# Kernel tuning notes

Hardware: AMD Instinct MI355X
Metric: run time of the kernel (lower is better)

## Reference

```python
import jax, jax.numpy as jnp
import numpy as np

EPS = 1e-5
K = 3  # neighborhood kernel size per axis


def setup_inputs() -> dict:
    key = jax.random.key(0)
    ks = jax.random.split(key, 12)
    C, F, G = 128, 512, 8
    s = 0.02
    d = {}
    d["x"] = jax.random.normal(ks[0], (1, C, 32, 32, 32), jnp.float32)
    d["qkv_w"] = s * jax.random.normal(ks[1], (3 * C, C), jnp.float32)
    d["qkv_b"] = jnp.zeros((3 * C,), jnp.float32)
    d["proj_w"] = s * jax.random.normal(ks[2], (C, C), jnp.float32)
    d["proj_b"] = jnp.zeros((C,), jnp.float32)
    d["rpb"] = s * jax.random.normal(ks[3], (G, 2 * K - 1, 2 * K - 1, 2 * K - 1), jnp.float32)
    d["w1"] = s * jax.random.normal(ks[4], (C, F), jnp.float32)
    d["b1"] = jnp.zeros((F,), jnp.float32)
    d["w2"] = s * jax.random.normal(ks[5], (F, C), jnp.float32)
    d["b2"] = jnp.zeros((C,), jnp.float32)
    return d


def _nb_idx(n, k):
    # NATTEN-style clamped window: neighborhood start clipped so the full
    # k-window stays in-bounds -> every query has exactly k neighbors per axis.
    pos = jnp.arange(n)
    start = jnp.clip(pos - (k // 2), 0, n - k)
    return start[:, None] + jnp.arange(k)[None, :]  # (n, k)


def _inorm(x):
    # InstanceNorm3d, affine=False: normalize each (b, c) over spatial dims
    m = jnp.mean(x, axis=(2, 3, 4), keepdims=True)
    v = jnp.var(x, axis=(2, 3, 4), keepdims=True)
    return (x - m) * jax.lax.rsqrt(v + EPS)


def _forward(x, qkv_w, qkv_b, proj_w, proj_b, rpb, w1, b1, w2, b2):
    b, c, h, w, z = x.shape
    G = rpb.shape[0]
    D = c // G

    # --- SAM: 3D neighborhood self-attention ---
    qkv = jnp.einsum('bchwz,oc->bohwz', x, qkv_w) + qkv_b[None, :, None, None, None]
    q, k_, v = jnp.split(qkv, 3, axis=1)
    q = q.reshape(b, G, D, h, w, z)
    k_ = k_.reshape(b, G, D, h, w, z)
    v = v.reshape(b, G, D, h, w, z)

    ih, iw, iz = _nb_idx(h, K), _nb_idx(w, K), _nb_idx(z, K)  # (h,K),(w,K),(z,K)
    IH = ih[:, None, None, :, None, None]
    IW = iw[None, :, None, None, :, None]
    IZ = iz[None, None, :, None, None, :]
    # gathered neighbors: (b, G, D, h, w, z, K, K, K) -> (..., K^3)
    knb = k_[:, :, :, IH, IW, IZ].reshape(b, G, D, h, w, z, K ** 3)
    vnb = v[:, :, :, IH, IW, IZ].reshape(b, G, D, h, w, z, K ** 3)

    # relative-position-bias indices in [0, 2K-2]
    rh = ih - jnp.arange(h)[:, None] + (K - 1)
    rw = iw - jnp.arange(w)[:, None] + (K - 1)
    rz = iz - jnp.arange(z)[:, None] + (K - 1)
    RH = rh[:, None, None, :, None, None]
    RW = rw[None, :, None, None, :, None]
    RZ = rz[None, None, :, None, None, :]
    rpbg = rpb[:, RH, RW, RZ].reshape(G, h, w, z, K ** 3)

    scale = D ** -0.5
    attn = jnp.einsum('bgdhwz,bgdhwzk->bghwzk', q, knb) * scale + rpbg[None]
    attn = jax.nn.softmax(attn, axis=-1)
    sam = jnp.einsum('bghwzk,bgdhwzk->bgdhwz', attn, vnb).reshape(b, c, h, w, z)
    sam = jnp.einsum('bchwz,oc->bohwz', sam, proj_w) + proj_b[None, :, None, None, None]

    # --- norm_in + FFN (tokens = h*w*z) + norm_out + residual + maxpool ---
    xn = _inorm(sam)
    t = xn.reshape(b, c, -1).transpose(0, 2, 1)  # (b, N, c)
    t = t + (jnp.matmul(jax.nn.relu(jnp.matmul(t, w1) + b1), w2) + b2)
    xn = _inorm(t.transpose(0, 2, 1).reshape(b, c, h, w, z))
    skip = xn + x
    down = jax.lax.reduce_window(skip, -jnp.inf, jax.lax.max,
                                 (1, 1, 2, 2, 2), (1, 1, 2, 2, 2), 'VALID')
    return down, skip


def reference(x, qkv_w, qkv_b, proj_w, proj_b, rpb, w1, b1, w2, b2):
    return _forward(x, qkv_w, qkv_b, proj_w, proj_b, rpb, w1, b1, w2, b2)
```

## Files before the change

### kernel.cpp

```cpp
#include <hip/hip_runtime.h>

#define NSP 32768
#define EPS 1e-5f

typedef __attribute__((ext_vector_type(8))) __bf16 bf16x8;
typedef __attribute__((ext_vector_type(4))) float f32x4;
typedef __attribute__((ext_vector_type(2))) float f32x2;
typedef __attribute__((ext_vector_type(8))) unsigned short us8;
typedef __attribute__((ext_vector_type(2))) unsigned short us2;

union U8 { us8 u; bf16x8 b; };

__device__ __forceinline__ unsigned short f2bf(float f) {
    unsigned u = __float_as_uint(f);
    u += 0x7fff + ((u >> 16) & 1);
    return (unsigned short)(u >> 16);
}
__device__ __forceinline__ float bf2f(unsigned short h) {
    return __uint_as_float(((unsigned)h) << 16);
}

__device__ __forceinline__ void prep_range(
    const float* __restrict__ W, int sO, int sC, int ntk,
    unsigned short* __restrict__ Wsw, int i)
{
    int tile = i >> 13;
    int s = i & 8191;
    int r = s >> 6;
    int byte = (s & 63) << 1;
    int ub = byte ^ ((r & 7) << 4);
    int c = ub >> 4;
    int j = (ub >> 1) & 7;
    int ob = tile / ntk;
    int ks = tile - ob * ntk;
    Wsw[i] = f2bf(W[(ob * 128 + r) * sO + (ks * 64 + c * 8 + j) * sC]);
}

__global__ __launch_bounds__(256) void prep_all(
    const float* __restrict__ qkv_w, const float* __restrict__ proj_w,
    const float* __restrict__ w1, const float* __restrict__ w2,
    unsigned short* __restrict__ qkv_sw, unsigned short* __restrict__ proj_sw,
    unsigned short* __restrict__ w1_sw, unsigned short* __restrict__ w2_sw,
    float* __restrict__ sums)
{
    int bid = blockIdx.x, tid = threadIdx.x;
    if (bid < 192)       prep_range(qkv_w, 128, 1, 2, qkv_sw, bid * 256 + tid);
    else if (bid < 256)  prep_range(proj_w, 128, 1, 2, proj_sw, (bid - 192) * 256 + tid);
    else if (bid < 512)  prep_range(w1, 1, 512, 2, w1_sw, (bid - 256) * 256 + tid);
    else if (bid < 768)  prep_range(w2, 1, 128, 8, w2_sw, (bid - 512) * 256 + tid);
    else { sums[tid] = 0.f; sums[tid + 256] = 0.f; }
}

template<int BN, int XMODE, int OMODE>
__global__ __launch_bounds__(256) void gemm_mfma(
    const unsigned short* __restrict__ Wsw,
    const void* __restrict__ X,
    const float* __restrict__ bias,
    const unsigned short* __restrict__ resid,
    const f32x2* __restrict__ table,
    void* __restrict__ Out,
    int K, int do_relu, int rw)
{
    constexpr int NF = BN / 32;
    constexpr int BCH = BN / 32;
    __shared__ __align__(16) unsigned short smem[8192 + BN * 64];
    unsigned short* Asm = smem;
    unsigned short* Bsm = smem + 8192;
    const int tid  = threadIdx.x;
    const int lane = tid & 63;
    const int wid  = tid >> 6;
    const int wr   = wid >> 1, wc = wid & 1;
    const int n0   = blockIdx.x * BN;
    const int o0   = blockIdx.y << 7;
    const int nk   = K >> 6;

    f32x4 acc[4][NF];
    #pragma unroll
    for (int m = 0; m < 4; ++m)
        #pragma unroll
        for (int n = 0; n < NF; ++n)
            acc[m][n] = (f32x4){0.f, 0.f, 0.f, 0.f};

    const int r  = (BN == 128) ? (tid & 127) : (tid & 63);
    const int kh = (BN == 128) ? (tid >> 7)  : (tid >> 6);

    us8 a_pre[4];
    us8 b_pre[BCH];
    int b_c[BCH];
    #pragma unroll
    for (int i = 0; i < BCH; ++i)
        b_c[i] = (BN == 128) ? (((((r >> 5) + i) & 3) << 1) + kh)
                             : (((((r >> 4) + i) & 1) << 2) + kh);

    auto load_tile = [&](int ks) {
        const char* gbase = (const char*)(Wsw + (size_t)(blockIdx.y * nk + ks) * 8192);
        #pragma unroll
        for (int i = 0; i < 4; ++i)
            a_pre[i] = *(const us8*)(gbase + i * 4096 + tid * 16);
        #pragma unroll
        for (int i = 0; i < BCH; ++i) {
            int c = b_c[i];
            int kb = (ks << 6) + (c << 3);
            us8 bv;
            if (XMODE == 0) {
                const float* xp = (const float*)X + (size_t)kb * NSP + n0 + r;
                #pragma unroll
                for (int j = 0; j < 8; ++j) bv[j] = f2bf(xp[(size_t)j * NSP]);
            } else if (XMODE == 2) {
                bv = *(const us8*)((const unsigned short*)X + (size_t)(n0 + r) * rw + kb);
            } else {
                const unsigned short* xp = (const unsigned short*)X + (size_t)kb * NSP + n0 + r;
                #pragma unroll
                for (int j = 0; j < 8; ++j) {
                    f32x2 t = table[kb + j];
                    bv[j] = f2bf((bf2f(xp[(size_t)j * NSP]) - t.x) * t.y);
                }
            }
            b_pre[i] = bv;
        }
    };
    auto store_tile = [&]() {
        #pragma unroll
        for (int i = 0; i < 4; ++i)
            *(us8*)((char*)Asm + i * 4096 + tid * 16) = a_pre[i];
        #pragma unroll
        for (int i = 0; i < BCH; ++i) {
            int off = (r << 7) + ((b_c[i] << 4) ^ ((r & 7) << 4));
            *(us8*)((char*)Bsm + off) = b_pre[i];
        }
    };

    load_tile(0);
    store_tile();
    __syncthreads();

    for (int ks = 0; ks < nk; ++ks) {
        if (ks + 1 < nk) load_tile(ks + 1);
        #pragma unroll
        for (int ki = 0; ki < 2; ++ki) {
            bf16x8 af[4], bfr[NF];
            int chunk = (ki << 2) + (lane >> 4);
            #pragma unroll
            for (int m = 0; m < 4; ++m) {
                int row = (wr << 6) + (m << 4) + (lane & 15);
                int off = (row << 7) + ((chunk << 4) ^ ((row & 7) << 4));
                U8 t; t.u = *(const us8*)((const char*)Asm + off);
                af[m] = t.b;
            }
            #pragma unroll
            for (int n = 0; n < NF; ++n) {
                int row = wc * (BN / 2) + (n << 4) + (lane & 15);
                int off = (row << 7) + ((chunk << 4) ^ ((row & 7) << 4));
                U8 t; t.u = *(const us8*)((const char*)Bsm + off);
                bfr[n] = t.b;
            }
            #pragma unroll
            for (int m = 0; m < 4; ++m)
                #pragma unroll
                for (int n = 0; n < NF; ++n)
                    acc[m][n] = __builtin_amdgcn_mfma_f32_16x16x32_bf16(af[m], bfr[n], acc[m][n], 0, 0, 0);
        }
        if (ks + 1 < nk) {
            __syncthreads();
            store_tile();
            __syncthreads();
        }
    }

    if (OMODE == 2 || OMODE == 3) {
        __syncthreads();
        unsigned short* Wt = smem + (wid << 12);
        #pragma unroll
        for (int m = 0; m < 4; ++m)
            #pragma unroll
            for (int reg = 0; reg < 4; ++reg) {
                int ol = (m << 4) + ((lane >> 4) << 2) + reg;
                float b = bias[o0 + (wr << 6) + ol];
                #pragma unroll
                for (int n = 0; n < NF; ++n) {
                    int cl = (n << 4) + (lane & 15);
                    float v = acc[m][n][reg] + b;
                    if (do_relu) v = fmaxf(v, 0.f);
                    Wt[ol * 64 + (cl ^ ((ol & 7) << 3))] = f2bf(v);
                }
            }
        const int d = lane & 15, coff = lane >> 4;
        unsigned short* O = (unsigned short*)Out;
        #pragma unroll
        for (int go = 0; go < 4; ++go) {
            #pragma unroll
            for (int cc = 0; cc < 16; ++cc) {
                int cl = (cc << 2) + coff;
                int ol = (go << 4) + d;
                unsigned short v = Wt[ol * 64 + (cl ^ ((ol & 7) << 3))];
                size_t idx;
                if (OMODE == 2) {
                    int g = (wr << 2) + go;
                    idx = ((size_t)((blockIdx.y << 3) + g) * NSP + n0 + (wc << 6) + cl) * 16 + d;
                } else {
                    idx = (size_t)(n0 + (wc << 6) + cl) * rw + o0 + (wr << 6) + (go << 4) + d;
                }
                O[idx] = v;
            }
        }
        return;
    }

    #pragma unroll
    for (int m = 0; m < 4; ++m) {
        #pragma unroll
        for (int reg = 0; reg < 4; ++reg) {
            int o = o0 + (wr << 6) + (m << 4) + ((lane >> 4) << 2) + reg;
            float b = bias[o];
            f32x2 rt = resid ? table[o] : (f32x2){0.f, 1.f};
            #pragma unroll
            for (int n = 0; n < NF; ++n) {
                int col = n0 + wc * (BN / 2) + (n << 4) + (lane & 15);
                size_t oi = (size_t)o * NSP + col;
                float v = acc[m][n][reg] + b;
                if (resid) v += (bf2f(resid[oi]) - rt.x) * rt.y;
                if (do_relu) v = fmaxf(v, 0.f);
                ((unsigned short*)Out)[oi] = f2bf(v);
            }
        }
    }
}

__global__ __launch_bounds__(256) void attn_kernel(
    const unsigned short* __restrict__ qkvT, const float* __restrict__ rpb,
    unsigned short* __restrict__ samT)
{
    const int g = blockIdx.y;
    const int n = blockIdx.x * 256 + threadIdx.x;
    const int h = n >> 10, w = (n >> 5) & 31, z = n & 31;
    const int ih0 = min(max(h - 1, 0), 29);
    const int iw0 = min(max(w - 1, 0), 29);
    const int iz0 = min(max(z - 1, 0), 29);

    const us8* qp = (const us8*)(qkvT + ((size_t)g * NSP + n) * 16);
    const unsigned short* kb = qkvT + (size_t)(8 + g) * NSP * 16;
    const unsigned short* vb = qkvT + (size_t)(16 + g) * NSP * 16;

    float q[16];
    {
        us8 q0 = qp[0], q1 = qp[1];
        #pragma unroll
        for (int j = 0; j < 8; ++j) { q[j] = bf2f(q0[j]); q[8 + j] = bf2f(q1[j]); }
    }

    float logits[27];
    int idx = 0;
    #pragma unroll
    for (int kh = 0; kh < 3; ++kh)
    #pragma unroll
    for (int kw = 0; kw < 3; ++kw)
    #pragma unroll
    for (int kz = 0; kz < 3; ++kz) {
        int hh = ih0 + kh, ww = iw0 + kw, zz = iz0 + kz;
        int nb = (hh << 10) + (ww << 5) + zz;
        const us8* kp = (const us8*)(kb + (size_t)nb * 16);
        us8 k0 = kp[0], k1 = kp[1];
        float s = 0.f;
        #pragma unroll
        for (int j = 0; j < 8; ++j) s += q[j] * bf2f(k0[j]);
        #pragma unroll
        for (int j = 0; j < 8; ++j) s += q[8 + j] * bf2f(k1[j]);
        int rh = hh - h + 2, rw = ww - w + 2, rz = zz - z + 2;
        logits[idx++] = s * 0.25f + rpb[g * 125 + rh * 25 + rw * 5 + rz];
    }

    float mx = -1e30f;
    #pragma unroll
    for (int i = 0; i < 27; ++i) mx = fmaxf(mx, logits[i]);
    float sum = 0.f;
    #pragma unroll
    for (int i = 0; i < 27; ++i) { logits[i] = __expf(logits[i] - mx); sum += logits[i]; }
    float inv = 1.f / sum;

    float o[16] = {};
    idx = 0;
    #pragma unroll
    for (int kh = 0; kh < 3; ++kh)
    #pragma unroll
    for (int kw = 0; kw < 3; ++kw)
    #pragma unroll
    for (int kz = 0; kz < 3; ++kz) {
        int nb = ((ih0 + kh) << 10) + ((iw0 + kw) << 5) + (iz0 + kz);
        const us8* vp = (const us8*)(vb + (size_t)nb * 16);
        us8 v0 = vp[0], v1 = vp[1];
        float a = logits[idx++] * inv;
        #pragma unroll
        for (int j = 0; j < 8; ++j) { o[j] += a * bf2f(v0[j]); o[8 + j] += a * bf2f(v1[j]); }
    }
    us8 o0v, o1v;
    #pragma unroll
    for (int j = 0; j < 8; ++j) { o0v[j] = f2bf(o[j]); o1v[j] = f2bf(o[8 + j]); }
    us8* op = (us8*)(samT + (size_t)n * 128 + g * 16);
    op[0] = o0v; op[1] = o1v;
}

__global__ __launch_bounds__(256) void inorm_partial_bf16(
    const unsigned short* __restrict__ in, float* __restrict__ sums)
{
    const int c = blockIdx.x >> 3, seg = blockIdx.x & 7;
    const us8* p = (const us8*)(in + (size_t)c * NSP + seg * 4096);
    float s = 0.f, ss = 0.f;
    #pragma unroll
    for (int i = 0; i < 2; ++i) {
        us8 v = p[threadIdx.x + i * 256];
        #pragma unroll
        for (int j = 0; j < 8; ++j) { float f = bf2f(v[j]); s += f; ss += f * f; }
    }
    for (int off = 32; off > 0; off >>= 1) {
        s  += __shfl_down(s, off);
        ss += __shfl_down(ss, off);
    }
    __shared__ float red[2][4];
    int wid = threadIdx.x >> 6;
    if ((threadIdx.x & 63) == 0) { red[0][wid] = s; red[1][wid] = ss; }
    __syncthreads();
    if (threadIdx.x == 0) {
        atomicAdd(&sums[c * 2],     red[0][0] + red[0][1] + red[0][2] + red[0][3]);
        atomicAdd(&sums[c * 2 + 1], red[1][0] + red[1][1] + red[1][2] + red[1][3]);
    }
}

__global__ void finalize_sums(const float* __restrict__ sums, f32x2* __restrict__ table)
{
    int c = threadIdx.x;
    float m = sums[c * 2] * (1.f / NSP);
    float var = sums[c * 2 + 1] * (1.f / NSP) - m * m;
    table[c] = (f32x2){m, rsqrtf(var + EPS)};
}

__global__ __launch_bounds__(256) void inorm_skip_pool(
    const unsigned short* __restrict__ t2, const float* __restrict__ x,
    const float* __restrict__ sums,
    float* __restrict__ skip, float* __restrict__ down)
{
    int m = blockIdx.x * 256 + threadIdx.x;
    int c = m >> 12;
    int r = m & 4095;
    int oh = r >> 8, ow = (r >> 4) & 15, oz = r & 15;
    float mean = sums[c * 2] * (1.f / NSP);
    float inv = rsqrtf(sums[c * 2 + 1] * (1.f / NSP) - mean * mean + EPS);
    size_t base = (size_t)c * NSP + oh * 2048 + ow * 64 + oz * 2;
    float mx = -1e30f;
    #pragma unroll
    for (int dh = 0; dh < 2; ++dh)
    #pragma unroll
    for (int dw = 0; dw < 2; ++dw) {
        size_t a = base + dh * 1024 + dw * 32;
        us2 tv = *(const us2*)(t2 + a);
        f32x2 xv = *(const f32x2*)(x + a);
        f32x2 sv;
        sv.x = (bf2f(tv.x) - mean) * inv + xv.x;
        sv.y = (bf2f(tv.y) - mean) * inv + xv.y;
        *(f32x2*)(skip + a) = sv;
        mx = fmaxf(mx, fmaxf(sv.x, sv.y));
    }
    down[m] = mx;
}

extern "C" void kernel_launch(void* const* d_in, const int* in_sizes, int n_in,
                              void* d_out, int out_size, void* d_ws, size_t ws_size,
                              hipStream_t stream)
{
    const float* x      = (const float*)d_in[0];
    const float* qkv_w  = (const float*)d_in[1];
    const float* qkv_b  = (const float*)d_in[2];
    const float* proj_w = (const float*)d_in[3];
    const float* proj_b = (const float*)d_in[4];
    const float* rpb    = (const float*)d_in[5];
    const float* w1     = (const float*)d_in[6];
    const float* b1     = (const float*)d_in[7];
    const float* w2     = (const float*)d_in[8];
    const float* b2     = (const float*)d_in[9];

    float* out  = (float*)d_out;
    float* down = out;
    float* skip = out + 524288;

    unsigned short* wb      = (unsigned short*)d_out;
    unsigned short* qkv_sw  = wb;
    unsigned short* proj_sw = wb + 49152;
    unsigned short* w1_sw   = wb + 65536;
    unsigned short* w2_sw   = wb + 131072;

    char* ws = (char*)d_ws;
    const size_t MB = 1u << 20;
    unsigned short* qkvT    = (unsigned short*)(ws);
    unsigned short* samT    = (unsigned short*)(ws + 24 * MB);
    unsigned short* yb      = (unsigned short*)(ws + 32 * MB);
    unsigned short* hiddenT = (unsigned short*)(ws);
    unsigned short* t2b     = (unsigned short*)(ws + 48 * MB);
    float*          sums    = (float*)(ws + 72 * MB);
    f32x2*          table1  = (f32x2*)(ws + 72 * MB + 4096);
    float* sums1 = sums;
    float* sums2 = sums + 256;

    prep_all<<<769, 256, 0, stream>>>(qkv_w, proj_w, w1, w2,
                                      qkv_sw, proj_sw, w1_sw, w2_sw, sums);

    gemm_mfma<128, 0, 2><<<dim3(256, 3), 256, 0, stream>>>(
        qkv_sw, x, qkv_b, nullptr, nullptr, qkvT, 128, 0, 0);
    attn_kernel<<<dim3(128, 8), 256, 0, stream>>>(qkvT, rpb, samT);
    gemm_mfma<64, 2, 1><<<dim3(512, 1), 256, 0, stream>>>(
        proj_sw, samT, proj_b, nullptr, nullptr, yb, 128, 0, 128);
    inorm_partial_bf16<<<1024, 256, 0, stream>>>(yb, sums1);
    finalize_sums<<<1, 128, 0, stream>>>(sums1, table1);
    gemm_mfma<128, 3, 3><<<dim3(256, 4), 256, 0, stream>>>(
        w1_sw, yb, b1, nullptr, table1, hiddenT, 128, 1, 512);
    gemm_mfma<64, 2, 1><<<dim3(512, 1), 256, 0, stream>>>(
        w2_sw, hiddenT, b2, yb, table1, t2b, 512, 0, 512);
    inorm_partial_bf16<<<1024, 256, 0, stream>>>(t2b, sums2);
    inorm_skip_pool<<<2048, 256, 0, stream>>>(t2b, x, sums2, skip, down);
}
```

Baseline: 191.0 us.

## Fuse FFN up and down projections into one MLP kernel keeping hidden in LDS

Replaces the two FFN GEMM launches and the finalize_sums kernel with a single mlp_kernel. Each block handles 64 tokens, normalizes its input tile in LDS, and loops over four 128-wide hidden chunks, computing relu(W1·x) into LDS and accumulating W2·h in registers, then adds the residual. This removes the global write and read of the 32768x512 bf16 hidden tensor and two launches. In exchange, each block reloads all weights from global or L2 memory, runs more sync barriers, and uses 64 KB of LDS, which may limit occupancy.

```diff
diff --git a/kernel.cpp b/kernel.cpp
--- a/kernel.cpp
+++ b/kernel.cpp
@@ -56,10 +56,8 @@
     const unsigned short* __restrict__ Wsw,
     const void* __restrict__ X,
     const float* __restrict__ bias,
-    const unsigned short* __restrict__ resid,
-    const f32x2* __restrict__ table,
     void* __restrict__ Out,
-    int K, int do_relu, int rw)
+    int K, int rw)
 {
     constexpr int NF = BN / 32;
     constexpr int BCH = BN / 32;
@@ -106,15 +104,8 @@
                 const float* xp = (const float*)X + (size_t)kb * NSP + n0 + r;
                 #pragma unroll
                 for (int j = 0; j < 8; ++j) bv[j] = f2bf(xp[(size_t)j * NSP]);
-            } else if (XMODE == 2) {
+            } else {
                 bv = *(const us8*)((const unsigned short*)X + (size_t)(n0 + r) * rw + kb);
-            } else {
-                const unsigned short* xp = (const unsigned short*)X + (size_t)kb * NSP + n0 + r;
-                #pragma unroll
-                for (int j = 0; j < 8; ++j) {
-                    f32x2 t = table[kb + j];
-                    bv[j] = f2bf((bf2f(xp[(size_t)j * NSP]) - t.x) * t.y);
-                }
             }
             b_pre[i] = bv;
         }
@@ -167,7 +158,7 @@
         }
     }
 
-    if (OMODE == 2 || OMODE == 3) {
+    if (BN == 128 && OMODE == 2) {
         __syncthreads();
         unsigned short* Wt = smem + (wid << 12);
         #pragma unroll
@@ -179,27 +170,20 @@
                 #pragma unroll
                 for (int n = 0; n < NF; ++n) {
                     int cl = (n << 4) + (lane & 15);
-                    float v = acc[m][n][reg] + b;
-                    if (do_relu) v = fmaxf(v, 0.f);
-                    Wt[ol * 64 + (cl ^ ((ol & 7) << 3))] = f2bf(v);
+                    Wt[ol * 64 + (cl ^ ((ol & 7) << 3))] = f2bf(acc[m][n][reg] + b);
                 }
             }
         const int d = lane & 15, coff = lane >> 4;
         unsigned short* O = (unsigned short*)Out;
         #pragma unroll
         for (int go = 0; go < 4; ++go) {
+            int g = (wr << 2) + go;
             #pragma unroll
             for (int cc = 0; cc < 16; ++cc) {
                 int cl = (cc << 2) + coff;
                 int ol = (go << 4) + d;
                 unsigned short v = Wt[ol * 64 + (cl ^ ((ol & 7) << 3))];
-                size_t idx;
-                if (OMODE == 2) {
-                    int g = (wr << 2) + go;
-                    idx = ((size_t)((blockIdx.y << 3) + g) * NSP + n0 + (wc << 6) + cl) * 16 + d;
-                } else {
-                    idx = (size_t)(n0 + (wc << 6) + cl) * rw + o0 + (wr << 6) + (go << 4) + d;
-                }
+                size_t idx = ((size_t)((blockIdx.y << 3) + g) * NSP + n0 + (wc << 6) + cl) * 16 + d;
                 O[idx] = v;
             }
         }
@@ -212,18 +196,170 @@
         for (int reg = 0; reg < 4; ++reg) {
             int o = o0 + (wr << 6) + (m << 4) + ((lane >> 4) << 2) + reg;
             float b = bias[o];
-            f32x2 rt = resid ? table[o] : (f32x2){0.f, 1.f};
             #pragma unroll
             for (int n = 0; n < NF; ++n) {
                 int col = n0 + wc * (BN / 2) + (n << 4) + (lane & 15);
                 size_t oi = (size_t)o * NSP + col;
-                float v = acc[m][n][reg] + b;
-                if (resid) v += (bf2f(resid[oi]) - rt.x) * rt.y;
-                if (do_relu) v = fmaxf(v, 0.f);
-                ((unsigned short*)Out)[oi] = f2bf(v);
-            }
-        }
-    }
+                ((unsigned short*)Out)[oi] = f2bf(acc[m][n][reg] + b);
+            }
+        }
+    }
+}
+
+__global__ __launch_bounds__(256) void mlp_kernel(
+    const unsigned short* __restrict__ w1_sw,
+    const unsigned short* __restrict__ w2_sw,
+    const unsigned short* __restrict__ yb,
+    const float* __restrict__ sums1,
+    const float* __restrict__ b1, const float* __restrict__ b2,
+    unsigned short* __restrict__ t2b)
+{
+    __shared__ __align__(16) unsigned short smem[32768];
+    unsigned short* Asm = smem;
+    unsigned short* Xs  = smem + 16384;
+    unsigned short* Hs  = smem + 24576;
+    const int tid  = threadIdx.x;
+    const int lane = tid & 63;
+    const int wid  = tid >> 6;
+    const int wr   = wid >> 1, wc = wid & 1;
+    const int n0   = blockIdx.x << 6;
+
+    {
+        const int r = tid & 63, q = tid >> 6;
+        #pragma unroll
+        for (int i = 0; i < 4; ++i) {
+            int ch = q + (i << 2);
+            int k0 = ch << 3;
+            us8 bv;
+            #pragma unroll
+            for (int j = 0; j < 8; ++j) {
+                int k = k0 + j;
+                float mmean = sums1[k * 2] * (1.f / NSP);
+                float inv = rsqrtf(sums1[k * 2 + 1] * (1.f / NSP) - mmean * mmean + EPS);
+                bv[j] = f2bf((bf2f(yb[(size_t)k * NSP + n0 + r]) - mmean) * inv);
+            }
+            int off = ((ch >> 3) << 13) + (r << 7) + (((ch & 7) << 4) ^ ((r & 7) << 4));
+            *(us8*)((char*)Xs + off) = bv;
+        }
+    }
+    __syncthreads();
+
+    f32x4 acc2[4][2];
+    #pragma unroll
+    for (int m = 0; m < 4; ++m)
+        #pragma unroll
+        for (int n = 0; n < 2; ++n)
+            acc2[m][n] = (f32x4){0.f, 0.f, 0.f, 0.f};
+
+    for (int c = 0; c < 4; ++c) {
+        if (c) __syncthreads();
+        {
+            const char* g = (const char*)(w1_sw + (size_t)c * 16384);
+            #pragma unroll
+            for (int i = 0; i < 8; ++i)
+                *(us8*)((char*)Asm + i * 4096 + tid * 16) = *(const us8*)(g + i * 4096 + tid * 16);
+        }
+        __syncthreads();
+        f32x4 accH[4][2];
+        #pragma unroll
+        for (int m = 0; m < 4; ++m)
+            #pragma unroll
+            for (int n = 0; n < 2; ++n)
+                accH[m][n] = (f32x4){0.f, 0.f, 0.f, 0.f};
+        #pragma unroll
+        for (int kt = 0; kt < 2; ++kt) {
+            #pragma unroll
+            for (int ki = 0; ki < 2; ++ki) {
+                int chunk = (ki << 2) + (lane >> 4);
+                bf16x8 af[4], bfr[2];
+                #pragma unroll
+                for (int m = 0; m < 4; ++m) {
+                    int row = (wr << 6) + (m << 4) + (lane & 15);
+                    int off = (kt << 14) + (row << 7) + ((chunk << 4) ^ ((row & 7) << 4));
+                    U8 t; t.u = *(const us8*)((const char*)Asm + off);
+                    af[m] = t.b;
+                }
+                #pragma unroll
+                for (int n = 0; n < 2; ++n) {
+                    int row = (wc << 5) + (n << 4) + (lane & 15);
+                    int off = (kt << 13) + (row << 7) + ((chunk << 4) ^ ((row & 7) << 4));
+                    U8 t; t.u = *(const us8*)((const char*)Xs + off);
+                    bfr[n] = t.b;
+                }
+                #pragma unroll
+                for (int m = 0; m < 4; ++m)
+                    #pragma unroll
+                    for (int n = 0; n < 2; ++n)
+                        accH[m][n] = __builtin_amdgcn_mfma_f32_16x16x32_bf16(af[m], bfr[n], accH[m][n], 0, 0, 0);
+            }
+        }
+        #pragma unroll
+        for (int m = 0; m < 4; ++m)
+            #pragma unroll
+            for (int reg = 0; reg < 4; ++reg) {
+                int ol = (m << 4) + ((lane >> 4) << 2) + reg;
+                float bb = b1[(c << 7) + (wr << 6) + ol];
+                #pragma unroll
+                for (int n = 0; n < 2; ++n) {
+                    int row = (wc << 5) + (n << 4) + (lane & 15);
+                    float v = fmaxf(accH[m][n][reg] + bb, 0.f);
+                    int byte = (wr << 13) + (row << 7) + (((ol >> 3) << 4) ^ ((row & 7) << 4)) + ((ol & 7) << 1);
+                    *(unsigned short*)((char*)Hs + byte) = f2bf(v);
+                }
+            }
+        __syncthreads();
+        {
+            const char* g = (const char*)(w2_sw + (size_t)c * 16384);
+            #pragma unroll
+            for (int i = 0; i < 8; ++i)
+                *(us8*)((char*)Asm + i * 4096 + tid * 16) = *(const us8*)(g + i * 4096 + tid * 16);
+        }
+        __syncthreads();
+        #pragma unroll
+        for (int kt = 0; kt < 2; ++kt) {
+            #pragma unroll
+            for (int ki = 0; ki < 2; ++ki) {
+                int chunk = (ki << 2) + (lane >> 4);
+                bf16x8 af[4], bfr[2];
+                #pragma unroll
+                for (int m = 0; m < 4; ++m) {
+                    int row = (wr << 6) + (m << 4) + (lane & 15);
+                    int off = (kt << 14) + (row << 7) + ((chunk << 4) ^ ((row & 7) << 4));
+                    U8 t; t.u = *(const us8*)((const char*)Asm + off);
+                    af[m] = t.b;
+                }
+                #pragma unroll
+                for (int n = 0; n < 2; ++n) {
+                    int row = (wc << 5) + (n << 4) + (lane & 15);
+                    int off = (kt << 13) + (row << 7) + ((chunk << 4) ^ ((row & 7) << 4));
+                    U8 t; t.u = *(const us8*)((const char*)Hs + off);
+                    bfr[n] = t.b;
+                }
+                #pragma unroll
+                for (int m = 0; m < 4; ++m)
+                    #pragma unroll
+                    for (int n = 0; n < 2; ++n)
+                        acc2[m][n] = __builtin_amdgcn_mfma_f32_16x16x32_bf16(af[m], bfr[n], acc2[m][n], 0, 0, 0);
+            }
+        }
+    }
+
+    #pragma unroll
+    for (int m = 0; m < 4; ++m)
+        #pragma unroll
+        for (int reg = 0; reg < 4; ++reg) {
+            int o2 = (wr << 6) + (m << 4) + ((lane >> 4) << 2) + reg;
+            float bb = b2[o2];
+            #pragma unroll
+            for (int n = 0; n < 2; ++n) {
+                int nl = (wc << 5) + (n << 4) + (lane & 15);
+                int xbyte = ((o2 >> 6) << 13) + (nl << 7)
+                          + ((((o2 & 63) >> 3) << 4) ^ ((nl & 7) << 4)) + ((o2 & 7) << 1);
+                float resid = bf2f(*(const unsigned short*)((const char*)Xs + xbyte));
+                float v = acc2[m][n][reg] + bb + resid;
+                t2b[(size_t)o2 * NSP + n0 + nl] = f2bf(v);
+            }
+        }
 }
 
 __global__ __launch_bounds__(256) void attn_kernel(
@@ -323,14 +459,6 @@
         atomicAdd(&sums[c * 2],     red[0][0] + red[0][1] + red[0][2] + red[0][3]);
         atomicAdd(&sums[c * 2 + 1], red[1][0] + red[1][1] + red[1][2] + red[1][3]);
     }
-}
-
-__global__ void finalize_sums(const float* __restrict__ sums, f32x2* __restrict__ table)
-{
-    int c = threadIdx.x;
-    float m = sums[c * 2] * (1.f / NSP);
-    float var = sums[c * 2 + 1] * (1.f / NSP) - m * m;
-    table[c] = (f32x2){m, rsqrtf(var + EPS)};
 }
 
 __global__ __launch_bounds__(256) void inorm_skip_pool(
@@ -392,10 +520,8 @@
     unsigned short* qkvT    = (unsigned short*)(ws);
     unsigned short* samT    = (unsigned short*)(ws + 24 * MB);
     unsigned short* yb      = (unsigned short*)(ws + 32 * MB);
-    unsigned short* hiddenT = (unsigned short*)(ws);
     unsigned short* t2b     = (unsigned short*)(ws + 48 * MB);
     float*          sums    = (float*)(ws + 72 * MB);
-    f32x2*          table1  = (f32x2*)(ws + 72 * MB + 4096);
     float* sums1 = sums;
     float* sums2 = sums + 256;
 
@@ -403,16 +529,12 @@
                                       qkv_sw, proj_sw, w1_sw, w2_sw, sums);
 
     gemm_mfma<128, 0, 2><<<dim3(256, 3), 256, 0, stream>>>(
-        qkv_sw, x, qkv_b, nullptr, nullptr, qkvT, 128, 0, 0);
+        qkv_sw, x, qkv_b, qkvT, 128, 0);
     attn_kernel<<<dim3(128, 8), 256, 0, stream>>>(qkvT, rpb, samT);
     gemm_mfma<64, 2, 1><<<dim3(512, 1), 256, 0, stream>>>(
-        proj_sw, samT, proj_b, nullptr, nullptr, yb, 128, 0, 128);
+        proj_sw, samT, proj_b, yb, 128, 128);
     inorm_partial_bf16<<<1024, 256, 0, stream>>>(yb, sums1);
-    finalize_sums<<<1, 128, 0, stream>>>(sums1, table1);
-    gemm_mfma<128, 3, 3><<<dim3(256, 4), 256, 0, stream>>>(
-        w1_sw, yb, b1, nullptr, table1, hiddenT, 128, 1, 512);
-    gemm_mfma<64, 2, 1><<<dim3(512, 1), 256, 0, stream>>>(
-        w2_sw, hiddenT, b2, yb, table1, t2b, 512, 0, 512);
+    mlp_kernel<<<512, 256, 0, stream>>>(w1_sw, w2_sw, yb, sums1, b1, b2, t2b);
     inorm_partial_bf16<<<1024, 256, 0, stream>>>(t2b, sums2);
     inorm_skip_pool<<<2048, 256, 0, stream>>>(t2b, x, sums2, skip, down);
 }
```

Measured after the change: 158.9 us. -16.8%, faster.
